# Performance work log

Measured on AMD Instinct MI355X. Metric: run time of the kernel, lower is better.

The kernel has to match this reference:

```python
import math
import jax, jax.numpy as jnp
import numpy as np

# ---------------- static config ----------------
L_MAX = 3
DIM = (L_MAX + 1) ** 2            # 16 = dim of 0e+1o+2e+3o
N_NODES = 8000
N_EDGES = 128000                  # avg 16 neighbors / node
F = 32                            # num_features (irrep multiplicity)
S = 10                            # num_species
NB = 8                            # num bessel basis fns
HID = 64                          # radial MLP hidden width
RD_HID = 16                       # readout MLP hidden (16x0e)
R_MAX = 5.0
AVG_NEIGH = 16.0
MEAN, STD = -1.5, 2.0
E0 = -10.0                        # atomic energy offset per node

_f = math.factorial

def _sl(l):
    return slice(l * l, (l + 1) * (l + 1))

# ---------------- real Clebsch-Gordan / Wigner-3j tables ----------------
def _su2_cg(j1, j2, j3):
    C = np.zeros((2 * j1 + 1, 2 * j2 + 1, 2 * j3 + 1))
    for m1 in range(-j1, j1 + 1):
        for m2 in range(-j2, j2 + 1):
            m3 = m1 + m2
            if abs(m3) > j3:
                continue
            pref = (2 * j3 + 1) * _f(j3 + j1 - j2) * _f(j3 - j1 + j2) * _f(j1 + j2 - j3) / _f(j1 + j2 + j3 + 1)
            pref *= _f(j3 + m3) * _f(j3 - m3) * _f(j1 - m1) * _f(j1 + m1) * _f(j2 - m2) * _f(j2 + m2)
            pref = math.sqrt(pref)
            s = 0.0
            for k in range(max(0, j2 - j3 - m1, j1 - j3 + m2), min(j1 + j2 - j3, j1 - m1, j2 + m2) + 1):
                s += (-1) ** k / (_f(k) * _f(j1 + j2 - j3 - k) * _f(j1 - m1 - k) * _f(j2 + m2 - k) * _f(j3 - j2 + m1 + k) * _f(j3 - j1 - m2 + k))
            C[j1 + m1, j2 + m2, j3 + m3] = pref * s
    return C

def _q_r2c(l):
    # complex <- real spherical-harmonic change of basis (e3nn convention)
    q = np.zeros((2 * l + 1, 2 * l + 1), dtype=complex)
    for m in range(-l, 0):
        q[l + m, l + abs(m)] = 1 / math.sqrt(2)
        q[l + m, l - abs(m)] = -1j / math.sqrt(2)
    q[l, l] = 1.0
    for m in range(1, l + 1):
        q[l + m, l + abs(m)] = (-1) ** m / math.sqrt(2)
        q[l + m, l - abs(m)] = 1j * (-1) ** m / math.sqrt(2)
    return (-1j) ** l * q

def _w3j(l1, l2, l3):
    C = _su2_cg(l1, l2, l3).astype(complex)
    C = np.einsum('abc,ai,bj,ck->ijk', C, _q_r2c(l1), _q_r2c(l2), np.conj(_q_r2c(l3)))
    assert np.abs(C.imag).max() < 1e-8
    return np.real(C)

PATHS = [(l1, l2, l3) for l1 in range(L_MAX + 1) for l2 in range(L_MAX + 1)
         for l3 in range(L_MAX + 1) if abs(l1 - l2) <= l3 <= l1 + l2]
NP_PATHS = len(PATHS)  # 34 CG paths
_W3J_NP = {p: _w3j(*p) for p in PATHS}
W3J = {p: jnp.asarray(v, dtype=jnp.float32) for p, v in _W3J_NP.items()}

def _sh_scales():
    # constants making recursively-built SH component-normalized (|Y_l|^2 = 2l+1)
    v = np.array([0.2, -0.6, 0.7]); v = v / np.linalg.norm(v)
    ys = {1: math.sqrt(3.0) * v}
    sc = {}
    for l in range(2, L_MAX + 1):
        t = np.einsum('abc,a,b->c', _W3J_NP[(l - 1, 1, l)], ys[l - 1], ys[1])
        sc[l] = math.sqrt(2 * l + 1) / np.linalg.norm(t)
        ys[l] = sc[l] * t
    return sc
SH_SCALE = _sh_scales()

# ---------------- equivariant building blocks ----------------
def spherical_harmonics(vectors):
    r = jnp.linalg.norm(vectors, axis=-1, keepdims=True)
    u = vectors / jnp.maximum(r, 1e-9)
    y1 = math.sqrt(3.0) * u
    Y = jnp.concatenate([jnp.ones_like(u[:, :1]), y1], axis=-1)
    prev = y1
    for l in range(2, L_MAX + 1):
        cur = SH_SCALE[l] * jnp.einsum('abc,ea,eb->ec', W3J[(l - 1, 1, l)], prev, y1)
        Y = jnp.concatenate([Y, cur], axis=-1)
        prev = cur
    return Y  # [E, 16]

def radial_embedding(r):
    # Bessel basis * polynomial envelope (RadialEmbeddingBlock)
    x = r / R_MAX
    n = jnp.arange(1, NB + 1, dtype=r.dtype)
    b = math.sqrt(2.0 / R_MAX) * jnp.sin(jnp.pi * x[:, None] * n[None, :]) / jnp.maximum(r, 1e-9)[:, None]
    p = 5.0
    env = 1 - (p + 1) * (p + 2) / 2 * x ** p + p * (p + 2) * x ** (p + 1) - p * (p + 1) / 2 * x ** (p + 2)
    env = jnp.where(x < 1.0, env, 0.0)
    return b * env[:, None]  # [E, NB]

def _lin(x, w):
    # e3nn Linear: per-l channel mixing. x [N,F,DIM], w [L_MAX+1,F,F]
    return jnp.concatenate([jnp.einsum('nfa,fg->nga', x[:, :, _sl(l)], w[l]) for l in range(L_MAX + 1)], axis=-1)

def _tp_edge(xs, Y, rw):
    # radially-weighted CG tensor product of node feats with edge SH (InteractionBlock core)
    out = jnp.zeros_like(xs)
    for p, (l1, l2, l3) in enumerate(PATHS):
        t = jnp.einsum('abc,efa,eb->efc', W3J[(l1, l2, l3)], xs[:, :, _sl(l1)], Y[:, _sl(l2)])
        out = out.at[:, :, _sl(l3)].add(rw[:, p, :, None] * t)
    return out

def _tp_node(x, y):
    # channel-wise symmetric CG product (EquivariantProductBasisBlock contraction)
    out = jnp.zeros_like(x)
    for (l1, l2, l3) in PATHS:
        t = jnp.einsum('abc,nfa,nfb->nfc', W3J[(l1, l2, l3)], x[:, :, _sl(l1)], y[:, :, _sl(l2)])
        out = out.at[:, :, _sl(l3)].add(t / math.sqrt(2 * l3 + 1))
    return out

# ---------------- inputs ----------------
def setup_inputs() -> dict:
    key = jax.random.key(0)
    ks = iter(jax.random.split(key, 40))
    def nrm(shape, fan):
        return jax.random.normal(next(ks), shape, dtype=jnp.float32) / math.sqrt(fan)
    inp = {}
    inp['vectors'] = jax.random.normal(next(ks), (N_EDGES, 3), dtype=jnp.float32) * 1.5
    inp['node_z'] = jax.random.randint(next(ks), (N_NODES,), 0, S)
    inp['senders'] = jax.random.randint(next(ks), (N_EDGES,), 0, N_NODES)
    inp['receivers'] = jax.random.randint(next(ks), (N_EDGES,), 0, N_NODES)
    inp['embed'] = nrm((S, F), 1)
    for i in (0, 1):
        inp['r%d_w0' % i] = nrm((NB, HID), NB)
        inp['r%d_w1' % i] = nrm((HID, HID), HID)
        inp['r%d_w2' % i] = nrm((HID, NP_PATHS * F), HID)
        inp['up%d' % i] = nrm((L_MAX + 1, F, F), F)
        inp['post%d' % i] = nrm((L_MAX + 1, F, F), F)
        inp['pb%d' % i] = nrm((S, 3, F), 1)
        inp['pblin%d' % i] = nrm((L_MAX + 1, F, F), F)
    inp['sel0'] = nrm((S, L_MAX + 1, F, F), F)
    inp['ro0'] = nrm((F, 1), F)
    inp['res1'] = nrm((S, F, F), F)
    inp['ro1_a'] = nrm((F, RD_HID), F)
    inp['ro1_b'] = nrm((RD_HID, 1), RD_HID)
    return inp

# ---------------- forward ----------------
def reference(vectors, node_z, senders, receivers, embed,
              r0_w0, r0_w1, r0_w2, up0, post0, pb0, pblin0, sel0, ro0,
              r1_w0, r1_w1, r1_w2, up1, post1, pb1, pblin1, res1, ro1_a, ro1_b):
    N = node_z.shape[0]
    r = jnp.linalg.norm(vectors, axis=-1)
    Y = spherical_harmonics(vectors)
    rad = radial_embedding(r)
    # node embedding: scalars only
    feats = jnp.zeros((N, F, DIM), vectors.dtype).at[:, :, 0].set(embed[node_z])

    def interaction(feats, w0, w1, w2, wup, wpost):
        h = _lin(feats, wup)
        rw = (jax.nn.silu(jax.nn.silu(rad @ w0) @ w1) @ w2).reshape(-1, NP_PATHS, F)
        msgs = _tp_edge(h[senders], Y, rw)
        agg = jax.ops.segment_sum(msgs, receivers, num_segments=N) / AVG_NEIGH
        return _lin(agg, wpost)

    def product_basis(A, wpb, wlin, z):
        B2 = _tp_node(A, A)           # correlation order 2
        B3 = _tp_node(B2, A)          # correlation order 3
        w = wpb[z]                     # [N,3,F] per-species contraction weights
        out = w[:, 0, :, None] * A + w[:, 1, :, None] * B2 + w[:, 2, :, None] * B3
        return _lin(out, wlin)

    # ---- layer 0: selector tensor product, linear readout ----
    h = interaction(feats, r0_w0, r0_w1, r0_w2, up0, post0)
    wz = sel0[node_z]  # FullyConnectedTensorProduct with one-hot species == per-species linear
    h = jnp.concatenate([jnp.einsum('nfa,nfg->nga', h[:, :, _sl(l)], wz[:, l]) for l in range(L_MAX + 1)], axis=-1)
    feats = product_basis(h, pb0, pblin0, node_z)
    e0 = (feats[:, :, 0] @ ro0)[:, 0]

    # ---- layer 1 (last): residual to scalars, nonlinear readout ----
    resid = jnp.einsum('nf,nfg->ng', feats[:, :, 0], res1[node_z])
    h = interaction(feats, r1_w0, r1_w1, r1_w2, up1, post1)
    h = product_basis(h, pb1, pblin1, node_z)
    sc = h[:, :, 0] + resid  # last-layer target irreps = F x 0e
    e1 = (jax.nn.silu(sc @ ro1_a) @ ro1_b)[:, 0]

    node_energies = MEAN + STD * (e0 + e1) + E0
    return jnp.sum(node_energies)
```

## Files before the change

### kernel.cpp

```cpp
#include <hip/hip_runtime.h>
#include <math.h>

#define NF 32
#define NPATHS 34

typedef __attribute__((ext_vector_type(8))) short bf16x8;
typedef __attribute__((ext_vector_type(4))) float f32x4;
typedef __attribute__((ext_vector_type(2))) float f32x2;

__device__ __forceinline__ unsigned short f2bf(float v){
  unsigned u = __float_as_uint(v);
  u += 0x7fffu + ((u>>16)&1u);
  return (unsigned short)(u>>16);
}
__device__ __forceinline__ float bf2f(unsigned short h){
  return __uint_as_float(((unsigned)h)<<16);
}

struct PathTab { int l1[NPATHS]; int l2[NPATHS]; int l3[NPATHS]; };
constexpr PathTab mkpaths(){
  PathTab t{}; int n=0;
  for(int a=0;a<=3;a++)for(int b=0;b<=3;b++)for(int c=0;c<=3;c++){
    int lo = a>b ? a-b : b-a;
    if(c>=lo && c<=a+b){ t.l1[n]=a; t.l2[n]=b; t.l3[n]=c; n++; }
  }
  return t;
}
constexpr PathTab PT = mkpaths();

struct FactT { double v[22]; };
constexpr FactT mkfactT(){ FactT f{}; f.v[0]=1.0; for(int i=1;i<22;i++) f.v[i]=f.v[i-1]*(double)i; return f; }
constexpr FactT FT = mkfactT();
constexpr double cfact(int n){ return FT.v[n]; }

constexpr double csqrt(double x){
  if(x<=0.0) return 0.0;
  double g = x<1.0 ? 1.0 : x;
  for(int i=0;i<40;i++) g=0.5*(g+x/g);
  return g;
}

constexpr double su2cg(int j1,int j2,int j3,int m1,int m2){
  int m3=m1+m2;
  if(m3<-j3||m3>j3) return 0.0;
  double pref = (double)(2*j3+1)*cfact(j3+j1-j2)*cfact(j3-j1+j2)*cfact(j1+j2-j3)/cfact(j1+j2+j3+1);
  pref *= cfact(j3+m3)*cfact(j3-m3)*cfact(j1-m1)*cfact(j1+m1)*cfact(j2-m2)*cfact(j2+m2);
  pref = csqrt(pref);
  int k0=0; if(j2-j3-m1>k0)k0=j2-j3-m1; if(j1-j3+m2>k0)k0=j1-j3+m2;
  int k1=j1+j2-j3; if(j1-m1<k1)k1=j1-m1; if(j2+m2<k1)k1=j2+m2;
  double s=0.0;
  for(int k=k0;k<=k1;k++){
    double d = cfact(k)*cfact(j1+j2-j3-k)*cfact(j1-m1-k)*cfact(j2+m2-k)*cfact(j3-j2+m1+k)*cfact(j3-j1-m2+k);
    s += (k&1)? -1.0/d : 1.0/d;
  }
  return pref*s;
}

struct ccd { double x, y; };
constexpr ccd cqval(int l,int r,int col){
  const double is2 = 0.70710678118654752440;
  double re=0.0, im=0.0;
  if (r<l){ if (col==2*l-r) re=is2; else if (col==r) im=-is2; }
  else if (r==l){ if (col==l) re=1.0; }
  else { double s = ((r-l)&1)? -1.0:1.0;
         if (col==r) re=s*is2; else if (col==2*l-r) im=s*is2; }
  ccd v{re,im};
  switch(l&3){
    case 1: return ccd{ v.y, -v.x };
    case 2: return ccd{-v.x, -v.y };
    case 3: return ccd{-v.y,  v.x };
    default: return v;
  }
}

constexpr double w3entry(int l1,int l2,int l3,int i,int j,int k){
  double re=0.0;
  for(int a=0;a<2*l1+1;a++){
    ccd qa=cqval(l1,a,i); if(qa.x==0.0&&qa.y==0.0) continue;
    for(int b=0;b<2*l2+1;b++){
      ccd qb=cqval(l2,b,j); if(qb.x==0.0&&qb.y==0.0) continue;
      int m1=a-l1, m2=b-l2, m3=m1+m2;
      if(m3<-l3||m3>l3) continue;
      int c=m3+l3;
      double cg=su2cg(l1,l2,l3,m1,m2); if(cg==0.0) continue;
      ccd qc=cqval(l3,c,k); qc.y=-qc.y;
      if(qc.x==0.0&&qc.y==0.0) continue;
      ccd ab{qa.x*qb.x-qa.y*qb.y, qa.x*qb.y+qa.y*qb.x};
      re += cg*(ab.x*qc.x - ab.y*qc.y);
    }
  }
  return re;
}

template<int L1,int L2,int L3> struct W3Arr { float v[(2*L1+1)*(2*L2+1)*(2*L3+1)]; };
template<int L1,int L2,int L3> constexpr W3Arr<L1,L2,L3> mkW3(double scale){
  W3Arr<L1,L2,L3> r{};
  for(int i=0;i<2*L1+1;i++)
    for(int j=0;j<2*L2+1;j++)
      for(int k=0;k<2*L3+1;k++)
        r.v[(i*(2*L2+1)+j)*(2*L3+1)+k] = (float)(w3entry(L1,L2,L3,i,j,k)*scale);
  return r;
}
template<int L1,int L2,int L3> constexpr W3Arr<L1,L2,L3> W3V = mkW3<L1,L2,L3>(1.0);
template<int L1,int L2,int L3> constexpr W3Arr<L1,L2,L3> W3N = mkW3<L1,L2,L3>(1.0/csqrt(2.0*L3+1.0));

struct SCt { double sc2, sc3; };
constexpr SCt mksc(){
  double v0=0.2,v1=-0.6,v2=0.7;
  double nv=csqrt(v0*v0+v1*v1+v2*v2);
  double s3=csqrt(3.0);
  double y1[3]={s3*v0/nv, s3*v1/nv, s3*v2/nv};
  double t2[5]={0,0,0,0,0}; double n2=0.0;
  for(int c=0;c<5;c++){
    double s=0.0;
    for(int a=0;a<3;a++)for(int b=0;b<3;b++) s += w3entry(1,1,2,a,b,c)*y1[a]*y1[b];
    t2[c]=s; n2+=s*s;
  }
  double sc2=csqrt(5.0)/csqrt(n2);
  double y2[5]={sc2*t2[0],sc2*t2[1],sc2*t2[2],sc2*t2[3],sc2*t2[4]};
  double n3=0.0;
  for(int c=0;c<7;c++){
    double s=0.0;
    for(int a=0;a<5;a++)for(int b=0;b<3;b++) s += w3entry(2,1,3,a,b,c)*y2[a]*y1[b];
    n3+=s*s;
  }
  double sc3=csqrt(7.0)/csqrt(n3);
  return SCt{sc2,sc3};
}
constexpr SCt SCV = mksc();

template<bool NORM,int l1,int l2,int l3,int A,int B,int C>
__device__ __forceinline__ void w3term(const float* __restrict__ x, const float* __restrict__ y,
                                       float rv, float* __restrict__ acc){
  constexpr float w = NORM ? W3N<l1,l2,l3>.v[(A*(2*l2+1)+B)*(2*l3+1)+C]
                           : W3V<l1,l2,l3>.v[(A*(2*l2+1)+B)*(2*l3+1)+C];
  if constexpr (w!=0.0f)
    acc[l3*l3+C] = fmaf(w, x[l1*l1+A]*y[l2*l2+B]*rv, acc[l3*l3+C]);
}
template<bool NORM,int l1,int l2,int l3,int A,int B,int C>
__device__ __forceinline__ void w3loopC(const float* x,const float* y,float rv,float* acc){
  if constexpr (C<2*l3+1){
    w3term<NORM,l1,l2,l3,A,B,C>(x,y,rv,acc);
    w3loopC<NORM,l1,l2,l3,A,B,C+1>(x,y,rv,acc);
  }
}
template<bool NORM,int l1,int l2,int l3,int A,int B>
__device__ __forceinline__ void w3loopB(const float* x,const float* y,float rv,float* acc){
  if constexpr (B<2*l2+1){
    w3loopC<NORM,l1,l2,l3,A,B,0>(x,y,rv,acc);
    w3loopB<NORM,l1,l2,l3,A,B+1>(x,y,rv,acc);
  }
}
template<bool NORM,int l1,int l2,int l3,int A>
__device__ __forceinline__ void w3loopA(const float* x,const float* y,float rv,float* acc){
  if constexpr (A<2*l1+1){
    w3loopB<NORM,l1,l2,l3,A,0>(x,y,rv,acc);
    w3loopA<NORM,l1,l2,l3,A+1>(x,y,rv,acc);
  }
}

template<int P>
__device__ __forceinline__ void tpn_paths(const float* x,const float* y,float* o){
  if constexpr (P<NPATHS){
    constexpr int l1=PT.l1[P], l2=PT.l2[P], l3=PT.l3[P];
    w3loopA<true,l1,l2,l3,0>(x,y,1.0f,o);
    tpn_paths<P+1>(x,y,o);
  }
}

__device__ __forceinline__ float tpn_scalar(const float* x,const float* y){
  float o[1]={0.f};
  w3loopA<true,0,0,0,0>(x,y,1.0f,o);
  w3loopA<true,1,1,0,0>(x,y,1.0f,o);
  w3loopA<true,2,2,0,0>(x,y,1.0f,o);
  w3loopA<true,3,3,0,0>(x,y,1.0f,o);
  return o[0];
}

template<int l1,int l2,int l3,int A,int B>
constexpr bool anyNZ(){
  for(int c=0;c<2*l3+1;c++)
    if(W3V<l1,l2,l3>.v[(A*(2*l2+1)+B)*(2*l3+1)+c]!=0.0f) return true;
  return false;
}
template<int l1,int l2,int l3,int A,int B,int C>
__device__ __forceinline__ void w3C2(const f32x2 p, f32x2* __restrict__ S){
  constexpr float w = W3V<l1,l2,l3>.v[(A*(2*l2+1)+B)*(2*l3+1)+C];
  if constexpr (w!=0.0f) S[C] = p*w + S[C];
  if constexpr (C+1<2*l3+1) w3C2<l1,l2,l3,A,B,C+1>(p,S);
}
template<int l1,int l2,int l3,int A,int B>
__device__ __forceinline__ void w3B2(const f32x2* __restrict__ x,const f32x2* __restrict__ y,
                                     f32x2* __restrict__ S){
  if constexpr (anyNZ<l1,l2,l3,A,B>()){
    f32x2 p = x[l1*l1+A]*y[l2*l2+B];
    w3C2<l1,l2,l3,A,B,0>(p,S);
  }
  if constexpr (B+1<2*l2+1) w3B2<l1,l2,l3,A,B+1>(x,y,S);
}
template<int l1,int l2,int l3,int A>
__device__ __forceinline__ void w3A2(const f32x2* __restrict__ x,const f32x2* __restrict__ y,
                                     f32x2* __restrict__ S){
  w3B2<l1,l2,l3,A,0>(x,y,S);
  if constexpr (A+1<2*l1+1) w3A2<l1,l2,l3,A+1>(x,y,S);
}
template<bool L0,int P>
__device__ __forceinline__ void tp2(const f32x2* __restrict__ x,const f32x2* __restrict__ y,
                                    const unsigned short* __restrict__ rp,
                                    f32x2* __restrict__ acc){
  if constexpr (P<NPATHS){
    constexpr int l1=PT.l1[P], l2=PT.l2[P], l3=PT.l3[P];
    if constexpr (!(L0 && l1!=0)){
      f32x2 S[2*l3+1];
      #pragma unroll
      for(int c=0;c<2*l3+1;c++) S[c]=(f32x2){0.f,0.f};
      w3A2<l1,l2,l3,0>(x,y,S);
      f32x2 rv = { bf2f(rp[P*576]), bf2f(rp[P*576+4]) };
      #pragma unroll
      for(int c=0;c<2*l3+1;c++) acc[l3*l3+c] = rv*S[c] + acc[l3*l3+c];
    }
    tp2<L0,P+1>(x,y,rp,acc);
  }
}

__global__ __launch_bounds__(256) void k_count(
    const int* __restrict__ rcv, int* __restrict__ deg, int E)
{
  int e=blockIdx.x*256+threadIdx.x;
  if(e>=E) return;
  atomicAdd(&deg[rcv[e]],1);
}

#define SCAN_PER 32
__global__ __launch_bounds__(1024) void k_scan(
    const int* __restrict__ deg, int* __restrict__ row,
    int* __restrict__ cur, int N)
{
  __shared__ int part[1024];
  int t=threadIdx.x;
  int per=(N+1023)/1024; if(per>SCAN_PER) per=SCAN_PER;
  int base=t*per;
  int loc[SCAN_PER];
  int s=0;
  for(int i=0;i<per;i++){ int idx=base+i; int v=(idx<N)? deg[idx]:0; loc[i]=s; s+=v; }
  part[t]=s;
  __syncthreads();
  for(int off=1;off<1024;off<<=1){
    int v=(t>=off)? part[t-off]:0;
    __syncthreads();
    part[t]+=v;
    __syncthreads();
  }
  int ex=(t==0)?0:part[t-1];
  for(int i=0;i<per;i++){
    int idx=base+i;
    if(idx<N){ int r=ex+loc[i]; row[idx]=r; cur[idx]=r; }
  }
  if(t==1023) row[N]=part[1023];
}

__global__ __launch_bounds__(256) void k_fill(
    const int* __restrict__ rcv, int* __restrict__ cur,
    int* __restrict__ eid, int E)
{
  int e=blockIdx.x*256+threadIdx.x;
  if(e>=E) return;
  int pos=atomicAdd(&cur[rcv[e]],1);
  eid[pos]=e;
}

__global__ __launch_bounds__(256) void k_edge_setup(
    const float* __restrict__ vec, const int* __restrict__ snd,
    const int* __restrict__ eid, float* __restrict__ Y,
    float* __restrict__ rad, int* __restrict__ snd_s, int E)
{
  int j = blockIdx.x*256+threadIdx.x;
  if (j>=E) return;
  int e = eid[j];
  snd_s[j]=snd[e];
  float vx=vec[3*e], vy=vec[3*e+1], vz=vec[3*e+2];
  float r=sqrtf(vx*vx+vy*vy+vz*vz);
  float inv=1.0f/fmaxf(r,1e-9f);
  float y[16];
  y[0]=1.0f;
  const float s3=1.7320508075688772f;
  y[1]=s3*vx*inv; y[2]=s3*vy*inv; y[3]=s3*vz*inv;
  constexpr float sc2=(float)SCV.sc2, sc3=(float)SCV.sc3;
  {
    float t[16];
    #pragma unroll
    for(int c=0;c<16;c++) t[c]=0.f;
    w3loopA<false,1,1,2,0>(y,y,1.0f,t);
    #pragma unroll
    for(int c=0;c<5;c++) y[4+c]=sc2*t[4+c];
    w3loopA<false,2,1,3,0>(y,y,1.0f,t);
    #pragma unroll
    for(int c=0;c<7;c++) y[9+c]=sc3*t[9+c];
  }
  float4* Yp=(float4*)(Y+(size_t)j*16);
  Yp[0]=make_float4(y[0],y[1],y[2],y[3]);
  Yp[1]=make_float4(y[4],y[5],y[6],y[7]);
  Yp[2]=make_float4(y[8],y[9],y[10],y[11]);
  Yp[3]=make_float4(y[12],y[13],y[14],y[15]);
  float x = r*0.2f;
  float env=0.f;
  if (x<1.0f){
    float x2=x*x; float x4=x2*x2; float x5=x4*x;
    env = 1.0f - 21.0f*x5 + 35.0f*x5*x - 15.0f*x5*x2;
  }
  const float cb = 0.632455532033675866f;
  float base = inv*env*cb;
  #pragma unroll
  for(int n=1;n<=8;n++)
    rad[(size_t)j*8 + n-1] = base*sinf(3.14159265358979323846f * x * (float)n);
}

__global__ __launch_bounds__(256) void k_embed16(
    const float* __restrict__ embed, const float* __restrict__ up0,
    const int* __restrict__ z, unsigned short* __restrict__ hl16, int N)
{
  int t=blockIdx.x*256+threadIdx.x;
  int n=t>>5, g=t&31;
  if(n>=N) return;
  const float* ep=embed+z[n]*32;
  float a=0.f;
  #pragma unroll 8
  for(int f=0;f<32;f++) a=fmaf(ep[f],up0[(f<<5)+g],a);
  bf16x8 o0={(short)f2bf(a),0,0,0,0,0,0,0};
  bf16x8 o1={0,0,0,0,0,0,0,0};
  bf16x8* op=(bf16x8*)(hl16+(size_t)n*512+g*16);
  op[0]=o0; op[1]=o1;
}

__global__ __launch_bounds__(256) void k_radial(
    const float* __restrict__ rad, const float* __restrict__ w0,
    const float* __restrict__ w1, unsigned short* __restrict__ hid, int E)
{
  __shared__ float w0s[8*64];
  __shared__ float w1s[64*64];
  int tid=threadIdx.x;
  for(int i=tid;i<512;i+=256) w0s[i]=w0[i];
  for(int i=tid;i<4096;i+=256) w1s[i]=w1[i];
  __syncthreads();
  int e=blockIdx.x*256+tid;
  if(e>=E) return;
  const float4* rp=(const float4*)(rad+(size_t)e*8);
  float4 ra=rp[0], rb=rp[1];
  float rv[8]={ra.x,ra.y,ra.z,ra.w,rb.x,rb.y,rb.z,rb.w};
  float h1[64];
  #pragma unroll 8
  for(int j=0;j<64;j++){
    float a=0.f;
    #pragma unroll
    for(int i=0;i<8;i++) a=fmaf(rv[i],w0s[i*64+j],a);
    h1[j]=a/(1.f+__expf(-a));
  }
  unsigned short* hp = hid+(size_t)e*64;
  #pragma unroll 4
  for(int j=0;j<64;j++){
    float a=0.f;
    #pragma unroll
    for(int i=0;i<64;i++) a=fmaf(h1[i],w1s[i*64+j],a);
    hp[j]=f2bf(a/(1.f+__expf(-a)));
  }
}

__global__ __launch_bounds__(256) void k_prep(
    const float* __restrict__ w2a, const float* __restrict__ w2b,
    unsigned short* __restrict__ ta, unsigned short* __restrict__ tb,
    const float* __restrict__ post0, const float* __restrict__ sel0,
    float* __restrict__ comb)
{
  int t=blockIdx.x*256+threadIdx.x;
  const int C2=2*1088*64;
  if(t<C2){
    const float* src = (t<1088*64)? w2a : w2b;
    unsigned short* dst = (t<1088*64)? ta : tb;
    int u = (t<1088*64)? t : t-1088*64;
    int c=u>>6, k=u&63;
    dst[(size_t)c*64+k]=f2bf(src[(size_t)k*1088+c]);
  } else {
    int u=t-C2;
    if(u<10*4096){
      int z=u>>12, r=u&4095;
      int l=r>>10, e=(r>>5)&31, g=r&31;
      const float* pp=post0+l*1024+e*32;
      const float* sp=sel0+(size_t)z*4096+l*1024;
      float a=0.f;
      #pragma unroll 8
      for(int f=0;f<32;f++) a=fmaf(pp[f], sp[f*32+g], a);
      comb[(size_t)z*4096 + l*1024 + e*32 + g]=a;
    }
  }
}

template<bool L0>
__global__ __launch_bounds__(256,3) void k_tp_fused(
    const unsigned short* __restrict__ hlin, const float* __restrict__ Y,
    const unsigned short* __restrict__ hid, const unsigned short* __restrict__ w2t,
    const int* __restrict__ snd_s, unsigned short* __restrict__ msgs,
    int eb, int ecnt)
{
  constexpr int NT  = L0 ? 8 : 68;
  constexpr int PD  = L0 ? 4 : 34;
  __shared__ unsigned short rws[PD*32*18] __attribute__((aligned(16)));
  int tid=threadIdx.x;
  int lane=tid&63, wave=tid>>6;
  int m16=lane&15, quad=lane>>4;
  int el0=blockIdx.x*16;
  int f=tid&31;
  int hb=(tid>>5)&1;
  int le_base = wave + hb*8;
  int el_s0 = el0 + le_base;
  int el_s1 = el0 + le_base + 4;
  int s0 = (el_s0<ecnt)? snd_s[eb+el_s0] : 0;
  int s1 = (el_s1<ecnt)? snd_s[eb+el_s1] : 0;
  {
    const unsigned short* Ab = hid + (size_t)el0*64;
    bf16x8 a0 = *(const bf16x8*)(Ab + m16*64 + quad*8);
    bf16x8 a1 = *(const bf16x8*)(Ab + m16*64 + 32 + quad*8);
    #pragma unroll 2
    for(int nt=wave; nt<NT; nt+=4){
      int col = nt*16 + m16;
      bf16x8 b0 = *(const bf16x8*)(w2t + (size_t)col*64 + quad*8);
      bf16x8 b1 = *(const bf16x8*)(w2t + (size_t)col*64 + 32 + quad*8);
      f32x4 acc = (f32x4){0.f,0.f,0.f,0.f};
      acc = __builtin_amdgcn_mfma_f32_16x16x32_bf16(a0,b0,acc,0,0,0);
      acc = __builtin_amdgcn_mfma_f32_16x16x32_bf16(a1,b1,acc,0,0,0);
      int fc = col&31, P = col>>5;
      unsigned w0 = (unsigned)f2bf(acc[0]) | ((unsigned)f2bf(acc[1])<<16);
      unsigned w1 = (unsigned)f2bf(acc[2]) | ((unsigned)f2bf(acc[3])<<16);
      unsigned* wp = (unsigned*)(rws + (size_t)(P*32+fc)*18 + quad*4);
      wp[0]=w0; wp[1]=w1;
    }
  }
  __syncthreads();
  if(el_s0>=ecnt) return;
  bool okB = (el_s1<ecnt);
  size_t jA = (size_t)(eb+el_s0);
  size_t jB = okB ? (size_t)(eb+el_s1) : jA;
  f32x2 hs[16];
  if constexpr (L0){
    hs[0] = (f32x2){ bf2f(hlin[(size_t)s0*512 + f*16]),
                     bf2f(hlin[(size_t)s1*512 + f*16]) };
  } else {
    const bf16x8* hA = (const bf16x8*)(hlin + (size_t)s0*512 + f*16);
    const bf16x8* hB = (const bf16x8*)(hlin + (size_t)s1*512 + f*16);
    bf16x8 ha0=hA[0], ha1=hA[1], hb0=hB[0], hb1=hB[1];
    #pragma unroll
    for(int c=0;c<8;c++){
      hs[c]   = (f32x2){ bf2f((unsigned short)ha0[c]), bf2f((unsigned short)hb0[c]) };
      hs[8+c] = (f32x2){ bf2f((unsigned short)ha1[c]), bf2f((unsigned short)hb1[c]) };
    }
  }
  f32x2 yv[16];
  {
    const float4* yA=(const float4*)(Y+jA*16);
    const float4* yB=(const float4*)(Y+jB*16);
    float4 a0=yA[0],a1=yA[1],a2=yA[2],a3=yA[3];
    float4 b0=yB[0],b1=yB[1],b2=yB[2],b3=yB[3];
    yv[0]=(f32x2){a0.x,b0.x}; yv[1]=(f32x2){a0.y,b0.y}; yv[2]=(f32x2){a0.z,b0.z}; yv[3]=(f32x2){a0.w,b0.w};
    yv[4]=(f32x2){a1.x,b1.x}; yv[5]=(f32x2){a1.y,b1.y}; yv[6]=(f32x2){a1.z,b1.z}; yv[7]=(f32x2){a1.w,b1.w};
    yv[8]=(f32x2){a2.x,b2.x}; yv[9]=(f32x2){a2.y,b2.y}; yv[10]=(f32x2){a2.z,b2.z}; yv[11]=(f32x2){a2.w,b2.w};
    yv[12]=(f32x2){a3.x,b3.x}; yv[13]=(f32x2){a3.y,b3.y}; yv[14]=(f32x2){a3.z,b3.z}; yv[15]=(f32x2){a3.w,b3.w};
  }
  const unsigned short* rp = rws + f*18 + le_base;
  f32x2 acc[16];
  #pragma unroll
  for(int c=0;c<16;c++) acc[c]=(f32x2){0.f,0.f};
  tp2<L0,0>(hs,yv,rp,acc);
  {
    bf16x8 m0, m1;
    #pragma unroll
    for(int c=0;c<8;c++){
      m0[c]=(short)f2bf(acc[c].x*0.0625f);
      m1[c]=(short)f2bf(acc[8+c].x*0.0625f);
    }
    bf16x8* mp=(bf16x8*)(msgs+(size_t)el_s0*512+f*16);
    mp[0]=m0; mp[1]=m1;
  }
  if(okB){
    bf16x8 m0, m1;
    #pragma unroll
    for(int c=0;c<8;c++){
      m0[c]=(short)f2bf(acc[c].y*0.0625f);
      m1[c]=(short)f2bf(acc[8+c].y*0.0625f);
    }
    bf16x8* mp=(bf16x8*)(msgs+(size_t)el_s1*512+f*16);
    mp[0]=m0; mp[1]=m1;
  }
}

template<bool INIT>
__global__ __launch_bounds__(256) void k_seg_sum(
    const unsigned short* __restrict__ msgs, const int* __restrict__ row,
    float* __restrict__ agg, int eb, int ecnt, int N)
{
  int t=blockIdx.x*256+threadIdx.x;
  int n=t>>6, q=t&63;
  if(n>=N) return;
  int lo=row[n], hi=row[n+1];
  int a0 = lo>eb ? lo : eb;
  int a1e = eb+ecnt;
  int a1 = hi<a1e ? hi : a1e;
  if(!INIT && a0>=a1) return;
  float s[8];
  #pragma unroll
  for(int i=0;i<8;i++) s[i]=0.f;
  for(int j=a0;j<a1;j++){
    bf16x8 v=*(const bf16x8*)(msgs+(size_t)(j-eb)*512+q*8);
    #pragma unroll
    for(int i=0;i<8;i++) s[i]+=bf2f((unsigned short)v[i]);
  }
  float4* a0p=(float4*)(agg+(size_t)n*512+q*8);
  if(INIT){
    a0p[0]=make_float4(s[0],s[1],s[2],s[3]);
    a0p[1]=make_float4(s[4],s[5],s[6],s[7]);
  } else {
    float4 o0=a0p[0], o1=a0p[1];
    o0.x+=s[0]; o0.y+=s[1]; o0.z+=s[2]; o0.w+=s[3];
    o1.x+=s[4]; o1.y+=s[5]; o1.z+=s[6]; o1.w+=s[7];
    a0p[0]=o0; a0p[1]=o1;
  }
}

__global__ __launch_bounds__(256) void k_node0(
    const float* __restrict__ agg, const float* __restrict__ combw,
    const float* __restrict__ pb0, const float* __restrict__ pblin0,
    const float* __restrict__ ro0, const float* __restrict__ res1,
    const float* __restrict__ up1, const int* __restrict__ z,
    float* __restrict__ e0, float* __restrict__ resid,
    unsigned short* __restrict__ hl16, int N)
{
  __shared__ float sh1[8*512] __attribute__((aligned(16)));
  __shared__ float sh2[8*512] __attribute__((aligned(16)));
  int tid=threadIdx.x;
  int n0=tid>>5, g=tid&31;
  int n=blockIdx.x*8+n0;
  bool act=(n<N);
  int zz = act? z[n] : 0;
  if(act){
    const float* wp = combw + (size_t)zz*4096;
    const float* ip = agg + (size_t)n*512;
    float A[16];
    #pragma unroll
    for(int c=0;c<16;c++) A[c]=0.f;
    #pragma unroll 8
    for(int f=0;f<NF;f++){
      const float4* xp=(const float4*)(ip+f*16);
      float4 x0=xp[0],x1=xp[1],x2=xp[2],x3=xp[3];
      float w0v=wp[(f<<5)+g],w1v=wp[1024+(f<<5)+g],w2v=wp[2048+(f<<5)+g],w3v=wp[3072+(f<<5)+g];
      A[0]=fmaf(x0.x,w0v,A[0]);  A[1]=fmaf(x0.y,w1v,A[1]);  A[2]=fmaf(x0.z,w1v,A[2]);  A[3]=fmaf(x0.w,w1v,A[3]);
      A[4]=fmaf(x1.x,w2v,A[4]);  A[5]=fmaf(x1.y,w2v,A[5]);  A[6]=fmaf(x1.z,w2v,A[6]);  A[7]=fmaf(x1.w,w2v,A[7]);
      A[8]=fmaf(x2.x,w2v,A[8]);  A[9]=fmaf(x2.y,w3v,A[9]);  A[10]=fmaf(x2.z,w3v,A[10]);A[11]=fmaf(x2.w,w3v,A[11]);
      A[12]=fmaf(x3.x,w3v,A[12]);A[13]=fmaf(x3.y,w3v,A[13]);A[14]=fmaf(x3.z,w3v,A[14]);A[15]=fmaf(x3.w,w3v,A[15]);
    }
    float B2[16],B3[16];
    #pragma unroll
    for(int c=0;c<16;c++){ B2[c]=0.f; B3[c]=0.f; }
    tpn_paths<0>(A,A,B2);
    tpn_paths<0>(B2,A,B3);
    float wa=pb0[zz*96+g], wb=pb0[zz*96+32+g], wc=pb0[zz*96+64+g];
    #pragma unroll
    for(int c=0;c<16;c++) sh1[n0*512+g*16+c]=wa*A[c]+wb*B2[c]+wc*B3[c];
  }
  __syncthreads();
  if(act){
    float ft[16];
    #pragma unroll
    for(int c=0;c<16;c++) ft[c]=0.f;
    const float* wp=pblin0;
    #pragma unroll 8
    for(int f=0;f<NF;f++){
      const float4* xp=(const float4*)(sh1+n0*512+f*16);
      float4 x0=xp[0],x1=xp[1],x2=xp[2],x3=xp[3];
      float w0v=wp[(f<<5)+g],w1v=wp[1024+(f<<5)+g],w2v=wp[2048+(f<<5)+g],w3v=wp[3072+(f<<5)+g];
      ft[0]=fmaf(x0.x,w0v,ft[0]);  ft[1]=fmaf(x0.y,w1v,ft[1]);  ft[2]=fmaf(x0.z,w1v,ft[2]);  ft[3]=fmaf(x0.w,w1v,ft[3]);
      ft[4]=fmaf(x1.x,w2v,ft[4]);  ft[5]=fmaf(x1.y,w2v,ft[5]);  ft[6]=fmaf(x1.z,w2v,ft[6]);  ft[7]=fmaf(x1.w,w2v,ft[7]);
      ft[8]=fmaf(x2.x,w2v,ft[8]);  ft[9]=fmaf(x2.y,w3v,ft[9]);  ft[10]=fmaf(x2.z,w3v,ft[10]);ft[11]=fmaf(x2.w,w3v,ft[11]);
      ft[12]=fmaf(x3.x,w3v,ft[12]);ft[13]=fmaf(x3.y,w3v,ft[13]);ft[14]=fmaf(x3.z,w3v,ft[14]);ft[15]=fmaf(x3.w,w3v,ft[15]);
    }
    #pragma unroll
    for(int c=0;c<16;c++) sh2[n0*512+g*16+c]=ft[c];
  }
  __syncthreads();
  if(act){
    const float* wp=res1+(size_t)zz*1024;
    float a=0.f;
    #pragma unroll 8
    for(int f=0;f<32;f++) a=fmaf(sh2[n0*512+f*16], wp[(f<<5)+g], a);
    resid[(size_t)n*32+g]=a;
    if(g==0){
      float b=0.f;
      #pragma unroll 8
      for(int f=0;f<32;f++) b=fmaf(sh2[n0*512+f*16], ro0[f], b);
      e0[n]=b;
    }
    float acc[16];
    #pragma unroll
    for(int c=0;c<16;c++) acc[c]=0.f;
    const float* wp2=up1;
    #pragma unroll 8
    for(int f=0;f<NF;f++){
      const float4* xp=(const float4*)(sh2+n0*512+f*16);
      float4 x0=xp[0],x1=xp[1],x2=xp[2],x3=xp[3];
      float w0v=wp2[(f<<5)+g],w1v=wp2[1024+(f<<5)+g],w2v=wp2[2048+(f<<5)+g],w3v=wp2[3072+(f<<5)+g];
      acc[0]=fmaf(x0.x,w0v,acc[0]);  acc[1]=fmaf(x0.y,w1v,acc[1]);  acc[2]=fmaf(x0.z,w1v,acc[2]);  acc[3]=fmaf(x0.w,w1v,acc[3]);
      acc[4]=fmaf(x1.x,w2v,acc[4]);  acc[5]=fmaf(x1.y,w2v,acc[5]);  acc[6]=fmaf(x1.z,w2v,acc[6]);  acc[7]=fmaf(x1.w,w2v,acc[7]);
      acc[8]=fmaf(x2.x,w2v,acc[8]);  acc[9]=fmaf(x2.y,w3v,acc[9]);  acc[10]=fmaf(x2.z,w3v,acc[10]);acc[11]=fmaf(x2.w,w3v,acc[11]);
      acc[12]=fmaf(x3.x,w3v,acc[12]);acc[13]=fmaf(x3.y,w3v,acc[13]);acc[14]=fmaf(x3.z,w3v,acc[14]);acc[15]=fmaf(x3.w,w3v,acc[15]);
    }
    bf16x8 o0,o1;
    #pragma unroll
    for(int c=0;c<8;c++){ o0[c]=(short)f2bf(acc[c]); o1[c]=(short)f2bf(acc[8+c]); }
    bf16x8* op=(bf16x8*)(hl16+(size_t)n*512+g*16);
    op[0]=o0; op[1]=o1;
  }
}

__global__ __launch_bounds__(256) void k_node1(
    const float* __restrict__ agg, const float* __restrict__ post1,
    const float* __restrict__ pb1, const float* __restrict__ pblin1,
    const int* __restrict__ z, const float* __restrict__ resid,
    const float* __restrict__ e0a, const float* __restrict__ ro1a,
    const float* __restrict__ ro1b, float* __restrict__ out, int N)
{
  __shared__ float sh[8*32];
  __shared__ float sh2[8*32];
  __shared__ float red[8];
  int tid=threadIdx.x;
  int n0=tid>>5, g=tid&31;
  int n=blockIdx.x*8+n0;
  bool act=(n<N);
  if(act){
    const float* wp=post1;
    const float* ip=agg+(size_t)n*512;
    float A[16];
    #pragma unroll
    for(int c=0;c<16;c++) A[c]=0.f;
    #pragma unroll 8
    for(int f=0;f<NF;f++){
      const float4* xp=(const float4*)(ip+f*16);
      float4 x0=xp[0],x1=xp[1],x2=xp[2],x3=xp[3];
      float w0v=wp[(f<<5)+g],w1v=wp[1024+(f<<5)+g],w2v=wp[2048+(f<<5)+g],w3v=wp[3072+(f<<5)+g];
      A[0]=fmaf(x0.x,w0v,A[0]);  A[1]=fmaf(x0.y,w1v,A[1]);  A[2]=fmaf(x0.z,w1v,A[2]);  A[3]=fmaf(x0.w,w1v,A[3]);
      A[4]=fmaf(x1.x,w2v,A[4]);  A[5]=fmaf(x1.y,w2v,A[5]);  A[6]=fmaf(x1.z,w2v,A[6]);  A[7]=fmaf(x1.w,w2v,A[7]);
      A[8]=fmaf(x2.x,w2v,A[8]);  A[9]=fmaf(x2.y,w3v,A[9]);  A[10]=fmaf(x2.z,w3v,A[10]);A[11]=fmaf(x2.w,w3v,A[11]);
      A[12]=fmaf(x3.x,w3v,A[12]);A[13]=fmaf(x3.y,w3v,A[13]);A[14]=fmaf(x3.z,w3v,A[14]);A[15]=fmaf(x3.w,w3v,A[15]);
    }
    float B2[16];
    #pragma unroll
    for(int c=0;c<16;c++) B2[c]=0.f;
    tpn_paths<0>(A,A,B2);
    float B3_0=tpn_scalar(B2,A);
    int zz=z[n];
    float wa=pb1[zz*96+g], wb=pb1[zz*96+32+g], wc=pb1[zz*96+64+g];
    sh[n0*32+g]=wa*A[0]+wb*B2[0]+wc*B3_0;
  }
  __syncthreads();
  if(act){
    float a=0.f;
    #pragma unroll 8
    for(int f=0;f<32;f++) a=fmaf(sh[n0*32+f], pblin1[(f<<5)+g], a);
    sh2[n0*32+g]=a+resid[(size_t)n*32+g];
  }
  __syncthreads();
  if(g==0){
    float val=0.f;
    if(act){
      float e1=0.f;
      #pragma unroll
      for(int j=0;j<16;j++){
        float a=0.f;
        #pragma unroll
        for(int f=0;f<32;f++) a=fmaf(sh2[n0*32+f],ro1a[f*16+j],a);
        float s=a/(1.f+__expf(-a));
        e1=fmaf(s,ro1b[j],e1);
      }
      val=-1.5f+2.0f*(e0a[n]+e1)-10.0f;
    }
    red[n0]=val;
  }
  __syncthreads();
  if(tid==0){
    float s=0.f;
    #pragma unroll
    for(int i=0;i<8;i++) s+=red[i];
    atomicAdd(out,s);
  }
}

extern "C" void kernel_launch(void* const* d_in, const int* in_sizes, int n_in,
                              void* d_out, int out_size, void* d_ws, size_t ws_size,
                              hipStream_t stream)
{
  const float* vec   =(const float*)d_in[0];
  const int*   zarr  =(const int*)  d_in[1];
  const int*   snd   =(const int*)  d_in[2];
  const int*   rcv   =(const int*)  d_in[3];
  const float* embed =(const float*)d_in[4];
  const float* r0w0  =(const float*)d_in[5];
  const float* r0w1  =(const float*)d_in[6];
  const float* r0w2  =(const float*)d_in[7];
  const float* up0   =(const float*)d_in[8];
  const float* post0 =(const float*)d_in[9];
  const float* pb0   =(const float*)d_in[10];
  const float* pblin0=(const float*)d_in[11];
  const float* r1w0  =(const float*)d_in[12];
  const float* r1w1  =(const float*)d_in[13];
  const float* r1w2  =(const float*)d_in[14];
  const float* up1   =(const float*)d_in[15];
  const float* post1 =(const float*)d_in[16];
  const float* pb1   =(const float*)d_in[17];
  const float* pblin1=(const float*)d_in[18];
  const float* sel0  =(const float*)d_in[19];
  const float* ro0   =(const float*)d_in[20];
  const float* res1  =(const float*)d_in[21];
  const float* ro1a  =(const float*)d_in[22];
  const float* ro1b  =(const float*)d_in[23];

  const int E = in_sizes[0]/3;
  const int N = in_sizes[1];
  const int Epad = (E+63)&~63;

  char* ws=(char*)d_ws;
  size_t o=0;
  auto alloc=[&](size_t bytes)->char*{
    char* p=ws+o;
    o=(o+bytes+255)&~(size_t)255;
    return p;
  };
  int*   deg  =(int*)  alloc((size_t)N*4);
  int*   rowp =(int*)  alloc((size_t)(N+1)*4);
  int*   cur  =(int*)  alloc((size_t)N*4);
  int*   eid  =(int*)  alloc((size_t)E*4);
  int*   snd_s=(int*)  alloc((size_t)E*4);
  float* Yb   =(float*)alloc((size_t)E*16*4);
  float* radb =(float*)alloc((size_t)E*8*4);
  unsigned short* hidb=(unsigned short*)alloc((size_t)(Epad+16)*64*2);
  unsigned short* w2t0=(unsigned short*)alloc((size_t)1088*64*2);
  unsigned short* w2t1=(unsigned short*)alloc((size_t)1088*64*2);
  unsigned short* hl16=(unsigned short*)alloc((size_t)N*512*2);
  float* combw=(float*)alloc((size_t)10*4096*4);
  float* bufB =(float*)alloc((size_t)N*512*4);
  float* bufC =(float*)alloc((size_t)N*512*4);
  float* e0b  =(float*)alloc((size_t)N*4);
  float* residb=(float*)alloc((size_t)N*32*4);
  char*  dyn  = ws+o;
  size_t remain = ws_size>o ? ws_size-o : 0;

  dim3 tb(256);
  dim3 nblk((unsigned)((N*32+255)/256));
  dim3 n8blk((unsigned)((N+7)/8));
  dim3 eblk((unsigned)((E+255)/256));
  dim3 qblk((unsigned)((N*64+255)/256));

  hipMemsetAsync(deg,0,(size_t)N*4,stream);
  k_count<<<eblk,tb,0,stream>>>(rcv,deg,E);
  k_scan<<<dim3(1),dim3(1024),0,stream>>>(deg,rowp,cur,N);
  k_fill<<<eblk,tb,0,stream>>>(rcv,cur,eid,E);

  k_edge_setup<<<eblk,tb,0,stream>>>(vec,snd,eid,Yb,radb,snd_s,E);
  k_prep<<<dim3((2*1088*64+10*4096+255)/256),tb,0,stream>>>(r0w2,r1w2,w2t0,w2t1,post0,sel0,combw);
  k_embed16<<<nblk,tb,0,stream>>>(embed,up0,zarr,hl16,N);

  auto run_edges=[&](bool l0, const unsigned short* hlin, const unsigned short* w2t, float* agg){
    long rows = (long)(remain/1024);
    rows -= rows%64;
    if (rows>(long)Epad) rows=Epad;
    if (rows<64) rows=64;
    unsigned short* msgsb = (unsigned short*)dyn;
    for(long eb=0;eb<E;eb+=rows){
      long cnt = E-eb; if(cnt>rows) cnt=rows;
      dim3 g2((unsigned)((cnt+15)/16));
      if(l0) k_tp_fused<true ><<<g2,tb,0,stream>>>(hlin,Yb,hidb+(size_t)eb*64,w2t,snd_s,msgsb,(int)eb,(int)cnt);
      else   k_tp_fused<false><<<g2,tb,0,stream>>>(hlin,Yb,hidb+(size_t)eb*64,w2t,snd_s,msgsb,(int)eb,(int)cnt);
      if(eb==0) k_seg_sum<true ><<<qblk,tb,0,stream>>>(msgsb,rowp,agg,(int)eb,(int)cnt,N);
      else      k_seg_sum<false><<<qblk,tb,0,stream>>>(msgsb,rowp,agg,(int)eb,(int)cnt,N);
    }
  };

  k_radial<<<eblk,tb,0,stream>>>(radb,r0w0,r0w1,hidb,E);
  run_edges(true,hl16,w2t0,bufB);
  k_node0<<<n8blk,tb,0,stream>>>(bufB,combw,pb0,pblin0,ro0,res1,up1,zarr,e0b,residb,hl16,N);

  k_radial<<<eblk,tb,0,stream>>>(radb,r1w0,r1w1,hidb,E);
  run_edges(false,hl16,w2t1,bufC);
  hipMemsetAsync(d_out,0,4,stream);
  k_node1<<<n8blk,tb,0,stream>>>(bufC,post1,pb1,pblin1,zarr,residb,e0b,ro1a,ro1b,(float*)d_out,N);
}
```

Measured before the change: 604.5 us.

## Fuse segment-sum into tensor-product kernel via LDS run-length reduction and atomics

Messages are no longer written to a bf16 global buffer and summed by a separate seg_sum kernel. Each block stages its 16 edges' fp32 messages in LDS, then reduces runs of edges that share a receiver (edges are sorted by receiver) and atomically adds the partial sums into the zero-initialised aggregation buffer. This removes the message write and read-back along with a kernel launch per chunk. In exchange it adds float atomics, makes accumulation order nondeterministic, and enlarges LDS use, which may lower occupancy in the L0 variant.

```diff
diff --git a/kernel.cpp b/kernel.cpp
--- a/kernel.cpp
+++ b/kernel.cpp
@@ -271,13 +271,15 @@
 
 __global__ __launch_bounds__(256) void k_edge_setup(
     const float* __restrict__ vec, const int* __restrict__ snd,
-    const int* __restrict__ eid, float* __restrict__ Y,
-    float* __restrict__ rad, int* __restrict__ snd_s, int E)
+    const int* __restrict__ rcv, const int* __restrict__ eid,
+    float* __restrict__ Y, float* __restrict__ rad,
+    int* __restrict__ snd_s, int* __restrict__ rcv_s, int E)
 {
   int j = blockIdx.x*256+threadIdx.x;
   if (j>=E) return;
   int e = eid[j];
   snd_s[j]=snd[e];
+  rcv_s[j]=rcv[e];
   float vx=vec[3*e], vy=vec[3*e+1], vz=vec[3*e+2];
   float r=sqrtf(vx*vx+vy*vy+vz*vz);
   float inv=1.0f/fmaxf(r,1e-9f);
@@ -398,12 +400,16 @@
 __global__ __launch_bounds__(256,3) void k_tp_fused(
     const unsigned short* __restrict__ hlin, const float* __restrict__ Y,
     const unsigned short* __restrict__ hid, const unsigned short* __restrict__ w2t,
-    const int* __restrict__ snd_s, unsigned short* __restrict__ msgs,
-    int eb, int ecnt)
+    const int* __restrict__ snd_s, const int* __restrict__ rcv_s,
+    float* __restrict__ agg, int eb, int ecnt)
 {
   constexpr int NT  = L0 ? 8 : 68;
   constexpr int PD  = L0 ? 4 : 34;
-  __shared__ unsigned short rws[PD*32*18] __attribute__((aligned(16)));
+  constexpr int RWSU = PD*32*18;
+  constexpr int LMU  = 16*512*2;
+  constexpr int LDSU = RWSU > LMU ? RWSU : LMU;
+  __shared__ unsigned short rws[LDSU] __attribute__((aligned(16)));
+  __shared__ int r16v[16];
   int tid=threadIdx.x;
   int lane=tid&63, wave=tid>>6;
   int m16=lane&15, quad=lane>>4;
@@ -413,8 +419,10 @@
   int le_base = wave + hb*8;
   int el_s0 = el0 + le_base;
   int el_s1 = el0 + le_base + 4;
-  int s0 = (el_s0<ecnt)? snd_s[eb+el_s0] : 0;
-  int s1 = (el_s1<ecnt)? snd_s[eb+el_s1] : 0;
+  bool actA = el_s0<ecnt, okB = el_s1<ecnt;
+  int s0 = actA ? snd_s[eb+el_s0] : 0;
+  int s1 = okB  ? snd_s[eb+el_s1] : 0;
+  if(tid<16) r16v[tid] = (el0+tid<ecnt) ? rcv_s[eb+el0+tid] : -1;
   {
     const unsigned short* Ab = hid + (size_t)el0*64;
     bf16x8 a0 = *(const bf16x8*)(Ab + m16*64 + quad*8);
@@ -435,10 +443,8 @@
     }
   }
   __syncthreads();
-  if(el_s0>=ecnt) return;
-  bool okB = (el_s1<ecnt);
-  size_t jA = (size_t)(eb+el_s0);
-  size_t jB = okB ? (size_t)(eb+el_s1) : jA;
+  size_t jA = actA ? (size_t)(eb+el_s0) : 0;
+  size_t jB = okB  ? (size_t)(eb+el_s1) : 0;
   f32x2 hs[16];
   if constexpr (L0){
     hs[0] = (f32x2){ bf2f(hlin[(size_t)s0*512 + f*16]),
@@ -469,58 +475,31 @@
   #pragma unroll
   for(int c=0;c<16;c++) acc[c]=(f32x2){0.f,0.f};
   tp2<L0,0>(hs,yv,rp,acc);
-  {
-    bf16x8 m0, m1;
-    #pragma unroll
-    for(int c=0;c<8;c++){
-      m0[c]=(short)f2bf(acc[c].x*0.0625f);
-      m1[c]=(short)f2bf(acc[8+c].x*0.0625f);
-    }
-    bf16x8* mp=(bf16x8*)(msgs+(size_t)el_s0*512+f*16);
-    mp[0]=m0; mp[1]=m1;
+  __syncthreads();
+  float* lm = (float*)rws;
+  if(actA){
+    #pragma unroll
+    for(int c=0;c<16;c++) lm[(le_base*32+f)*16+c] = acc[c].x*0.0625f;
   }
   if(okB){
-    bf16x8 m0, m1;
-    #pragma unroll
-    for(int c=0;c<8;c++){
-      m0[c]=(short)f2bf(acc[c].y*0.0625f);
-      m1[c]=(short)f2bf(acc[8+c].y*0.0625f);
-    }
-    bf16x8* mp=(bf16x8*)(msgs+(size_t)el_s1*512+f*16);
-    mp[0]=m0; mp[1]=m1;
-  }
-}
-
-template<bool INIT>
-__global__ __launch_bounds__(256) void k_seg_sum(
-    const unsigned short* __restrict__ msgs, const int* __restrict__ row,
-    float* __restrict__ agg, int eb, int ecnt, int N)
-{
-  int t=blockIdx.x*256+threadIdx.x;
-  int n=t>>6, q=t&63;
-  if(n>=N) return;
-  int lo=row[n], hi=row[n+1];
-  int a0 = lo>eb ? lo : eb;
-  int a1e = eb+ecnt;
-  int a1 = hi<a1e ? hi : a1e;
-  if(!INIT && a0>=a1) return;
-  float s[8];
+    #pragma unroll
+    for(int c=0;c<16;c++) lm[((le_base+4)*32+f)*16+c] = acc[c].y*0.0625f;
+  }
+  __syncthreads();
   #pragma unroll
-  for(int i=0;i<8;i++) s[i]=0.f;
-  for(int j=a0;j<a1;j++){
-    bf16x8 v=*(const bf16x8*)(msgs+(size_t)(j-eb)*512+q*8);
-    #pragma unroll
-    for(int i=0;i<8;i++) s[i]+=bf2f((unsigned short)v[i]);
-  }
-  float4* a0p=(float4*)(agg+(size_t)n*512+q*8);
-  if(INIT){
-    a0p[0]=make_float4(s[0],s[1],s[2],s[3]);
-    a0p[1]=make_float4(s[4],s[5],s[6],s[7]);
-  } else {
-    float4 o0=a0p[0], o1=a0p[1];
-    o0.x+=s[0]; o0.y+=s[1]; o0.z+=s[2]; o0.w+=s[3];
-    o1.x+=s[4]; o1.y+=s[5]; o1.z+=s[6]; o1.w+=s[7];
-    a0p[0]=o0; a0p[1]=o1;
+  for(int s=tid; s<512; s+=256){
+    int ff=s>>4, cc=s&15;
+    float run=0.f; int cur=-1;
+    #pragma unroll
+    for(int le=0; le<16; le++){
+      int rr = r16v[le];
+      if(rr != cur){
+        if(cur >= 0) atomicAdd(agg + (size_t)cur*512 + s, run);
+        run = 0.f; cur = rr;
+      }
+      if(rr >= 0) run += lm[(le*32+ff)*16 + cc];
+    }
+    if(cur >= 0) atomicAdd(agg + (size_t)cur*512 + s, run);
   }
 }
 
@@ -735,6 +714,7 @@
   int*   cur  =(int*)  alloc((size_t)N*4);
   int*   eid  =(int*)  alloc((size_t)E*4);
   int*   snd_s=(int*)  alloc((size_t)E*4);
+  int*   rcv_s=(int*)  alloc((size_t)E*4);
   float* Yb   =(float*)alloc((size_t)E*16*4);
   float* radb =(float*)alloc((size_t)E*8*4);
   unsigned short* hidb=(unsigned short*)alloc((size_t)(Epad+16)*64*2);
@@ -746,38 +726,26 @@
   float* bufC =(float*)alloc((size_t)N*512*4);
   float* e0b  =(float*)alloc((size_t)N*4);
   float* residb=(float*)alloc((size_t)N*32*4);
-  char*  dyn  = ws+o;
-  size_t remain = ws_size>o ? ws_size-o : 0;
 
   dim3 tb(256);
   dim3 nblk((unsigned)((N*32+255)/256));
   dim3 n8blk((unsigned)((N+7)/8));
   dim3 eblk((unsigned)((E+255)/256));
-  dim3 qblk((unsigned)((N*64+255)/256));
+  dim3 e16blk((unsigned)((E+15)/16));
 
   hipMemsetAsync(deg,0,(size_t)N*4,stream);
   k_count<<<eblk,tb,0,stream>>>(rcv,deg,E);
   k_scan<<<dim3(1),dim3(1024),0,stream>>>(deg,rowp,cur,N);
   k_fill<<<eblk,tb,0,stream>>>(rcv,cur,eid,E);
 
-  k_edge_setup<<<eblk,tb,0,stream>>>(vec,snd,eid,Yb,radb,snd_s,E);
+  k_edge_setup<<<eblk,tb,0,stream>>>(vec,snd,rcv,eid,Yb,radb,snd_s,rcv_s,E);
   k_prep<<<dim3((2*1088*64+10*4096+255)/256),tb,0,stream>>>(r0w2,r1w2,w2t0,w2t1,post0,sel0,combw);
   k_embed16<<<nblk,tb,0,stream>>>(embed,up0,zarr,hl16,N);
 
   auto run_edges=[&](bool l0, const unsigned short* hlin, const unsigned short* w2t, float* agg){
-    long rows = (long)(remain/1024);
-    rows -= rows%64;
-    if (rows>(long)Epad) rows=Epad;
-    if (rows<64) rows=64;
-    unsigned short* msgsb = (unsigned short*)dyn;
-    for(long eb=0;eb<E;eb+=rows){
-      long cnt = E-eb; if(cnt>rows) cnt=rows;
-      dim3 g2((unsigned)((cnt+15)/16));
-      if(l0) k_tp_fused<true ><<<g2,tb,0,stream>>>(hlin,Yb,hidb+(size_t)eb*64,w2t,snd_s,msgsb,(int)eb,(int)cnt);
-      else   k_tp_fused<false><<<g2,tb,0,stream>>>(hlin,Yb,hidb+(size_t)eb*64,w2t,snd_s,msgsb,(int)eb,(int)cnt);
-      if(eb==0) k_seg_sum<true ><<<qblk,tb,0,stream>>>(msgsb,rowp,agg,(int)eb,(int)cnt,N);
-      else      k_seg_sum<false><<<qblk,tb,0,stream>>>(msgsb,rowp,agg,(int)eb,(int)cnt,N);
-    }
+    hipMemsetAsync(agg,0,(size_t)N*512*4,stream);
+    if(l0) k_tp_fused<true ><<<e16blk,tb,0,stream>>>(hlin,Yb,hidb,w2t,snd_s,rcv_s,agg,0,E);
+    else   k_tp_fused<false><<<e16blk,tb,0,stream>>>(hlin,Yb,hidb,w2t,snd_s,rcv_s,agg,0,E);
   };
 
   k_radial<<<eblk,tb,0,stream>>>(radb,r0w0,r0w1,hidb,E);
```

New measurement: 589.8 us. 1.02x faster.
